# Kernel optimization log

Measured on AMD Instinct MI355X. Metric: run time of the kernel, lower is better.

Reference implementation:

```python
import jax, jax.numpy as jnp
import numpy as np

STATIC_SEQ_DIM = 48  # STAT_DIM(27) + X_TIME_DIM(13) + 8
HIDDEN = 128


def setup_inputs() -> dict:
    key = jax.random.key(0)
    ks = jax.random.split(key, 8)
    B, T = 4096, 512

    def n(k, shape, scale):
        return jax.random.normal(k, shape, dtype=jnp.float32) * scale

    return {
        "y_flow": jax.random.normal(ks[0], (B, T, 1), dtype=jnp.float32),
        "x_statics": jax.random.normal(ks[1], (B, T, STATIC_SEQ_DIM), dtype=jnp.float32),
        "twin_idx": 256,
        "enc_w1": n(ks[2], (STATIC_SEQ_DIM, STATIC_SEQ_DIM), 0.1),
        "enc_b1": jnp.zeros((STATIC_SEQ_DIM,), jnp.float32),
        "enc_w2": n(ks[3], (STATIC_SEQ_DIM, STATIC_SEQ_DIM), 0.1),
        "enc_b2": jnp.zeros((STATIC_SEQ_DIM,), jnp.float32),
        "w_ih": n(ks[4], (4 * HIDDEN, 1 + STATIC_SEQ_DIM), 0.05),
        "w_hh": n(ks[5], (4 * HIDDEN, HIDDEN), 0.05),
        "b_ih": jnp.zeros((4 * HIDDEN,), jnp.float32),
        "b_hh": jnp.zeros((4 * HIDDEN,), jnp.float32),
        "out_w": n(ks[6], (1, HIDDEN), 0.05),
        "out_b": jnp.zeros((1,), jnp.float32),
    }


def reference(y_flow, x_statics, enc_w1, enc_b1, enc_w2, enc_b2,
              w_ih, w_hh, b_ih, b_hh, out_w, out_b, twin_idx):
    B, T, _ = y_flow.shape
    H = w_hh.shape[1]
    # Static encoder MLP has no cross-time dependency -> vectorize over (B, T-1)
    xs = x_statics[:, : T - 1]                                        # (B,T-1,S)
    enc = jax.nn.relu(xs @ enc_w1.T + enc_b1) @ enc_w2.T + enc_b2     # (B,T-1,S)
    enc_t = jnp.swapaxes(enc, 0, 1)                                   # (T-1,B,S)
    flow_t = jnp.swapaxes(y_flow[:, : T - 1], 0, 1)                   # (T-1,B,1)
    ts = jnp.arange(T - 1)

    def step(carry, x):
        h, c, last_pred = carry
        flow_teacher, e_t, t = x
        flow = jnp.where(t < twin_idx - 1, flow_teacher, last_pred)   # (B,1)
        x_in = jnp.concatenate([flow, e_t], axis=-1)                  # (B,1+S)
        gates = x_in @ w_ih.T + b_ih + h @ w_hh.T + b_hh              # (B,4H)
        i, f, g, o = jnp.split(gates, 4, axis=-1)                     # torch gate order
        c_new = jax.nn.sigmoid(f) * c + jax.nn.sigmoid(i) * jnp.tanh(g)
        h_new = jax.nn.sigmoid(o) * jnp.tanh(c_new)
        pred = h_new @ out_w.T + out_b                                # (B,1)
        return (h_new, c_new, pred), pred

    h0 = jnp.zeros((B, H), jnp.float32)
    c0 = jnp.zeros((B, H), jnp.float32)
    p0 = jnp.zeros((B, 1), jnp.float32)
    _, preds = jax.lax.scan(step, (h0, c0, p0), (flow_t, enc_t, ts))  # (T-1,B,1)
    return jnp.swapaxes(preds, 0, 1)                                  # (B,T-1,1)
```

## Files before the change

kernel.cpp:

```cpp
#include <hip/hip_runtime.h>
#include <hip/hip_bf16.h>

#define HID 128
#define SDIM 48
#define NSTEP 511
#define TFULL 512
#define ROWS 16
#define XHS 200
#define O1S 88
#define WENC_OFF 98304
#define BIAS_BYTE_OFF 208896

typedef unsigned short u16;
typedef unsigned int   u32;
typedef __attribute__((ext_vector_type(8))) short short8;
typedef __attribute__((ext_vector_type(4))) float f32x4;

__device__ __forceinline__ float frcp(float x)  { return __builtin_amdgcn_rcpf(x); }
__device__ __forceinline__ float sigm(float x)  { return frcp(1.0f + __expf(-x)); }
__device__ __forceinline__ float tanh_f(float x){ return 1.0f - 2.0f*frcp(1.0f + __expf(2.0f*x)); }
__device__ __forceinline__ u16 f2bf(float f) {
  __hip_bfloat16 h = __float2bfloat16(f);
  return *reinterpret_cast<u16*>(&h);
}
__device__ __forceinline__ u32 pk2(float a, float b) {
  return (u32)f2bf(a) | ((u32)f2bf(b) << 16);
}
__device__ __forceinline__ short8 pack8(float4 a, float4 b) {
  short8 r;
  r[0]=(short)f2bf(a.x); r[1]=(short)f2bf(a.y); r[2]=(short)f2bf(a.z); r[3]=(short)f2bf(a.w);
  r[4]=(short)f2bf(b.x); r[5]=(short)f2bf(b.y); r[6]=(short)f2bf(b.z); r[7]=(short)f2bf(b.w);
  return r;
}

__global__ void setup_weights(const float* __restrict__ w_ih, const float* __restrict__ w_hh,
                              const float* __restrict__ b_ih, const float* __restrict__ b_hh,
                              const float* __restrict__ enc_w1, const float* __restrict__ enc_w2,
                              u16* __restrict__ frags, float* __restrict__ bias) {
  int stride = gridDim.x * blockDim.x;
  int i0 = blockIdx.x * blockDim.x + threadIdx.x;
  for (int idx = i0; idx < 32*6*64*8; idx += stride) {
    int j  = idx & 7;
    int l  = (idx >> 3) & 63;
    int kt = (idx >> 9) % 6;
    int mt = (idx >> 9) / 6;
    int gr = mt*16 + (l & 15);
    int k  = kt*32 + (l >> 4)*8 + j;
    float v = 0.f;
    if (k < 48)       v = w_ih[gr*49 + 1 + k];
    else if (k < 176) v = w_hh[gr*HID + (k - 48)];
    frags[idx] = f2bf(v);
  }
  for (int idx = i0; idx < 2*3*2*64*8; idx += stride) {
    int j   = idx & 7;
    int l   = (idx >> 3) & 63;
    int kt  = (idx >> 9) & 1;
    int mt  = (idx >> 10) % 3;
    int lyr = (idx >> 10) / 3;
    int row = mt*16 + (l & 15);
    int k   = kt*32 + (l >> 4)*8 + j;
    float v = 0.f;
    if (k < SDIM) v = (lyr ? enc_w2 : enc_w1)[row*SDIM + k];
    frags[WENC_OFF + idx] = f2bf(v);
  }
  for (int idx = i0; idx < 512; idx += stride)
    bias[idx] = b_ih[idx] + b_hh[idx];
}

__global__ __launch_bounds__(512, 2)
void lstm_mfma(const float* __restrict__ y_flow,
               const float* __restrict__ x_statics,
               const int* __restrict__ twin_p,
               const float* __restrict__ enc_b1, const float* __restrict__ enc_b2,
               const float* __restrict__ out_w, const float* __restrict__ out_b,
               const float* __restrict__ w_ih,
               const u16* __restrict__ frags, const float* __restrict__ bias,
               float* __restrict__ out) {
  __shared__ __attribute__((aligned(16))) u16   s_xh[2][ROWS][XHS];
  __shared__ __attribute__((aligned(16))) u16   s_o1[ROWS][O1S];
  __shared__ __attribute__((aligned(16))) float s_pp[2][ROWS][8];
  __shared__ __attribute__((aligned(16))) float s_bias[512];
  __shared__ __attribute__((aligned(16))) float s_eb1[SDIM];
  __shared__ __attribute__((aligned(16))) float s_eb2[SDIM];

  const int tid = threadIdx.x;
  const int blk = blockIdx.x;
  const int w  = tid >> 6;
  const int l  = tid & 63;
  const int lr = l & 15;
  const int lg = l >> 4;
  const size_t b0 = (size_t)blk * ROWS;

  short8 wf[4][6];
  #pragma unroll
  for (int q = 0; q < 4; ++q)
    #pragma unroll
    for (int kt = 0; kt < 6; ++kt)
      wf[q][kt] = *(const short8*)(frags + (((w + 8*q)*6 + kt)*64 + l)*8);

  float wfl[4][4];
  #pragma unroll
  for (int q = 0; q < 4; ++q)
    #pragma unroll
    for (int r = 0; r < 4; ++r)
      wfl[q][r] = w_ih[((w + 8*q)*16 + lg*4 + r)*49];

  short8 we1[3][2], we2[3][2];
  if (w == 7) {
    #pragma unroll
    for (int mt = 0; mt < 3; ++mt)
      #pragma unroll
      for (int kt = 0; kt < 2; ++kt) {
        we1[mt][kt] = *(const short8*)(frags + WENC_OFF + (((0*3 + mt)*2 + kt)*64 + l)*8);
        we2[mt][kt] = *(const short8*)(frags + WENC_OFF + (((1*3 + mt)*2 + kt)*64 + l)*8);
      }
  }

  float owv[4];
  #pragma unroll
  for (int r = 0; r < 4; ++r) owv[r] = out_w[w*16 + lg*4 + r];
  const float ob  = out_b[0];
  const int   twc = twin_p[0] - 1;

  for (int i = tid; i < 2*ROWS*XHS; i += 512) ((u16*)s_xh)[i] = 0;
  for (int i = tid; i < ROWS*O1S;  i += 512) ((u16*)s_o1)[i] = 0;
  for (int i = tid; i < 2*ROWS*8;  i += 512) ((float*)s_pp)[i] = 0.f;
  s_bias[tid] = bias[tid];
  if (tid < SDIM) { s_eb1[tid] = enc_b1[tid]; s_eb2[tid] = enc_b2[tid]; }
  __syncthreads();

  const float* xrow = x_statics + (size_t)(b0 + lr)*TFULL*SDIM;
  const float* yrow = y_flow    + (size_t)(b0 + lr)*TFULL;

  auto enc_step = [&](short8 bx0, short8 bx1, int pp) {
    f32x4 a[3];
    #pragma unroll
    for (int mt = 0; mt < 3; ++mt) a[mt] = *(const f32x4*)&s_eb1[mt*16 + lg*4];
    #pragma unroll
    for (int mt = 0; mt < 3; ++mt) {
      a[mt] = __builtin_amdgcn_mfma_f32_16x16x32_bf16(we1[mt][0], bx0, a[mt], 0, 0, 0);
      a[mt] = __builtin_amdgcn_mfma_f32_16x16x32_bf16(we1[mt][1], bx1, a[mt], 0, 0, 0);
    }
    #pragma unroll
    for (int mt = 0; mt < 3; ++mt) {
      *(u32*)&s_o1[lr][mt*16 + lg*4]     = pk2(fmaxf(a[mt][0],0.f), fmaxf(a[mt][1],0.f));
      *(u32*)&s_o1[lr][mt*16 + lg*4 + 2] = pk2(fmaxf(a[mt][2],0.f), fmaxf(a[mt][3],0.f));
    }
    asm volatile("s_waitcnt lgkmcnt(0)" ::: "memory");
    __builtin_amdgcn_sched_barrier(0);
    short8 bo0 = *(const short8*)&s_o1[lr][lg*8];
    short8 bo1 = *(const short8*)&s_o1[lr][32 + lg*8];
    f32x4 e[3];
    #pragma unroll
    for (int mt = 0; mt < 3; ++mt) e[mt] = *(const f32x4*)&s_eb2[mt*16 + lg*4];
    #pragma unroll
    for (int mt = 0; mt < 3; ++mt) {
      e[mt] = __builtin_amdgcn_mfma_f32_16x16x32_bf16(we2[mt][0], bo0, e[mt], 0, 0, 0);
      e[mt] = __builtin_amdgcn_mfma_f32_16x16x32_bf16(we2[mt][1], bo1, e[mt], 0, 0, 0);
    }
    #pragma unroll
    for (int mt = 0; mt < 3; ++mt) {
      *(u32*)&s_xh[pp][lr][mt*16 + lg*4]     = pk2(e[mt][0], e[mt][1]);
      *(u32*)&s_xh[pp][lr][mt*16 + lg*4 + 2] = pk2(e[mt][2], e[mt][3]);
    }
  };

  float4 zf4 = make_float4(0.f, 0.f, 0.f, 0.f);
  float4 xn0a = zf4, xn0b = zf4, xn1a = zf4, xn1b = zf4;
  if (w == 7) {
    float4 c0a = *(const float4*)(xrow + lg*8);
    float4 c0b = *(const float4*)(xrow + lg*8 + 4);
    float4 c1a = zf4, c1b = zf4;
    if (lg < 2) {
      c1a = *(const float4*)(xrow + 32 + lg*8);
      c1b = *(const float4*)(xrow + 32 + lg*8 + 4);
    }
    enc_step(pack8(c0a, c0b), pack8(c1a, c1b), 0);
    xn0a = *(const float4*)(xrow + SDIM + lg*8);
    xn0b = *(const float4*)(xrow + SDIM + lg*8 + 4);
    if (lg < 2) {
      xn1a = *(const float4*)(xrow + SDIM + 32 + lg*8);
      xn1b = *(const float4*)(xrow + SDIM + 32 + lg*8 + 4);
    }
  }
  float c_reg[4] = {0.f, 0.f, 0.f, 0.f};
  __syncthreads();

  for (int st = 0; st < NSTEP; ++st) {
    const int p  = st & 1;
    const int p2 = p ^ 1;

    short8 bh[6];
    #pragma unroll
    for (int kt = 0; kt < 6; ++kt)
      bh[kt] = *(const short8*)&s_xh[p][lr][kt*32 + lg*8];

    f32x4 acc[4];
    #pragma unroll
    for (int q = 0; q < 4; ++q) acc[q] = *(const f32x4*)&s_bias[(w + 8*q)*16 + lg*4];
    #pragma unroll
    for (int kt = 0; kt < 6; ++kt)
      #pragma unroll
      for (int q = 0; q < 4; ++q)
        acc[q] = __builtin_amdgcn_mfma_f32_16x16x32_bf16(wf[q][kt], bh[kt], acc[q], 0, 0, 0);

    f32x4 pa = *(const f32x4*)&s_pp[p][lr][0];
    f32x4 pb = *(const f32x4*)&s_pp[p][lr][4];
    float pp_s = ((pa[0]+pa[1]) + (pa[2]+pa[3])) + ((pb[0]+pb[1]) + (pb[2]+pb[3]));
    float pred_prev = pp_s + ob;
    if (st == 0) pred_prev = 0.f;
    if (st > 0 && l < 16 && (l >> 1) == w)
      out[(b0 + l)*NSTEP + (st - 1)] = pred_prev;

    float tf = 0.f;
    if (st < twc) tf = yrow[st];
    const float flow = (st < twc) ? tf : pred_prev;

    if (w == 7) {
      short8 bx0 = pack8(xn0a, xn0b);
      short8 bx1 = pack8(xn1a, xn1b);
      const int tt = (st + 2 < TFULL) ? (st + 2) : (TFULL - 1);
      xn0a = *(const float4*)(xrow + (size_t)tt*SDIM + lg*8);
      xn0b = *(const float4*)(xrow + (size_t)tt*SDIM + lg*8 + 4);
      if (lg < 2) {
        xn1a = *(const float4*)(xrow + (size_t)tt*SDIM + 32 + lg*8);
        xn1b = *(const float4*)(xrow + (size_t)tt*SDIM + 32 + lg*8 + 4);
      }
      __builtin_amdgcn_s_setprio(1);
      enc_step(bx0, bx1, p2);
      __builtin_amdgcn_s_setprio(0);
    }

    float hv[4];
    float hsum = 0.f;
    #pragma unroll
    for (int r = 0; r < 4; ++r) {
      float g_i = acc[0][r] + wfl[0][r]*flow;
      float g_f = acc[1][r] + wfl[1][r]*flow;
      float g_g = acc[2][r] + wfl[2][r]*flow;
      float g_o = acc[3][r] + wfl[3][r]*flow;
      float iv = sigm(g_i);
      float fv = sigm(g_f);
      float gv = tanh_f(g_g);
      float ov = sigm(g_o);
      float c  = fv*c_reg[r] + iv*gv;
      c_reg[r] = c;
      hv[r] = ov*tanh_f(c);
      hsum += hv[r]*owv[r];
    }
    *(u32*)&s_xh[p2][lr][48 + w*16 + lg*4]     = pk2(hv[0], hv[1]);
    *(u32*)&s_xh[p2][lr][48 + w*16 + lg*4 + 2] = pk2(hv[2], hv[3]);
    hsum += __shfl_xor(hsum, 16);
    hsum += __shfl_xor(hsum, 32);
    if (l < 16) s_pp[p2][l][w] = hsum;
    __syncthreads();
  }

  f32x4 pa = *(const f32x4*)&s_pp[NSTEP & 1][lr][0];
  f32x4 pb = *(const f32x4*)&s_pp[NSTEP & 1][lr][4];
  float pp_s = ((pa[0]+pa[1]) + (pa[2]+pa[3])) + ((pb[0]+pb[1]) + (pb[2]+pb[3]));
  if (l < 16 && (l >> 1) == w)
    out[(b0 + l)*NSTEP + (NSTEP - 1)] = pp_s + ob;
}

extern "C" void kernel_launch(void* const* d_in, const int* in_sizes, int n_in,
                              void* d_out, int out_size, void* d_ws, size_t ws_size,
                              hipStream_t stream) {
  const float* y_flow    = (const float*)d_in[0];
  const float* x_statics = (const float*)d_in[1];
  const int*   twin      = (const int*)  d_in[2];
  const float* enc_w1    = (const float*)d_in[3];
  const float* enc_b1    = (const float*)d_in[4];
  const float* enc_w2    = (const float*)d_in[5];
  const float* enc_b2    = (const float*)d_in[6];
  const float* w_ih      = (const float*)d_in[7];
  const float* w_hh      = (const float*)d_in[8];
  const float* b_ih      = (const float*)d_in[9];
  const float* b_hh      = (const float*)d_in[10];
  const float* out_w     = (const float*)d_in[11];
  const float* out_b     = (const float*)d_in[12];
  float* out = (float*)d_out;

  char* ws = (char*)d_ws;
  u16*   frags = (u16*)ws;
  float* bias  = (float*)(ws + BIAS_BYTE_OFF);

  setup_weights<<<128, 256, 0, stream>>>(w_ih, w_hh, b_ih, b_hh, enc_w1, enc_w2, frags, bias);
  lstm_mfma<<<256, 512, 0, stream>>>(y_flow, x_statics, twin,
                                     enc_b1, enc_b2, out_w, out_b, w_ih,
                                     frags, bias, out);
}
```

Baseline: 802.4 us.

## Split static encoder across two waves and break MFMA accumulator chains

Encoder layer 1 moves to wave 6 and layer 2 to wave 7, with a double-buffered intermediate between them, so the encoder runs as a two-stage pipeline. This takes the serialized two-layer MLP off a single wave's critical path in each recurrent step. The gate GEMM now splits the K loop into two independent accumulator sets, which shortens the dependent MFMA chain at the cost of extra adds and registers. The prediction partial sums are also transposed to a [wave][row] layout, and the enc_L1 parameter named `ob` shadows the outer out_b variable of the same name.

```diff
diff --git a/kernel.cpp b/kernel.cpp
--- a/kernel.cpp
+++ b/kernel.cpp
@@ -77,8 +77,8 @@
                const u16* __restrict__ frags, const float* __restrict__ bias,
                float* __restrict__ out) {
   __shared__ __attribute__((aligned(16))) u16   s_xh[2][ROWS][XHS];
-  __shared__ __attribute__((aligned(16))) u16   s_o1[ROWS][O1S];
-  __shared__ __attribute__((aligned(16))) float s_pp[2][ROWS][8];
+  __shared__ __attribute__((aligned(16))) u16   s_o1[2][ROWS][O1S];
+  __shared__ __attribute__((aligned(16))) float s_pp[2][8][ROWS];
   __shared__ __attribute__((aligned(16))) float s_bias[512];
   __shared__ __attribute__((aligned(16))) float s_eb1[SDIM];
   __shared__ __attribute__((aligned(16))) float s_eb2[SDIM];
@@ -106,7 +106,7 @@
       wfl[q][r] = w_ih[((w + 8*q)*16 + lg*4 + r)*49];
 
   short8 we1[3][2], we2[3][2];
-  if (w == 7) {
+  if (w >= 6) {
     #pragma unroll
     for (int mt = 0; mt < 3; ++mt)
       #pragma unroll
@@ -123,8 +123,8 @@
   const int   twc = twin_p[0] - 1;
 
   for (int i = tid; i < 2*ROWS*XHS; i += 512) ((u16*)s_xh)[i] = 0;
-  for (int i = tid; i < ROWS*O1S;  i += 512) ((u16*)s_o1)[i] = 0;
-  for (int i = tid; i < 2*ROWS*8;  i += 512) ((float*)s_pp)[i] = 0.f;
+  for (int i = tid; i < 2*ROWS*O1S; i += 512) ((u16*)s_o1)[i] = 0;
+  for (int i = tid; i < 2*8*ROWS;  i += 512) ((float*)s_pp)[i] = 0.f;
   s_bias[tid] = bias[tid];
   if (tid < SDIM) { s_eb1[tid] = enc_b1[tid]; s_eb2[tid] = enc_b2[tid]; }
   __syncthreads();
@@ -132,7 +132,7 @@
   const float* xrow = x_statics + (size_t)(b0 + lr)*TFULL*SDIM;
   const float* yrow = y_flow    + (size_t)(b0 + lr)*TFULL;
 
-  auto enc_step = [&](short8 bx0, short8 bx1, int pp) {
+  auto enc_L1 = [&](short8 bx0, short8 bx1, int ob) {
     f32x4 a[3];
     #pragma unroll
     for (int mt = 0; mt < 3; ++mt) a[mt] = *(const f32x4*)&s_eb1[mt*16 + lg*4];
@@ -143,13 +143,13 @@
     }
     #pragma unroll
     for (int mt = 0; mt < 3; ++mt) {
-      *(u32*)&s_o1[lr][mt*16 + lg*4]     = pk2(fmaxf(a[mt][0],0.f), fmaxf(a[mt][1],0.f));
-      *(u32*)&s_o1[lr][mt*16 + lg*4 + 2] = pk2(fmaxf(a[mt][2],0.f), fmaxf(a[mt][3],0.f));
-    }
-    asm volatile("s_waitcnt lgkmcnt(0)" ::: "memory");
-    __builtin_amdgcn_sched_barrier(0);
-    short8 bo0 = *(const short8*)&s_o1[lr][lg*8];
-    short8 bo1 = *(const short8*)&s_o1[lr][32 + lg*8];
+      *(u32*)&s_o1[ob][lr][mt*16 + lg*4]     = pk2(fmaxf(a[mt][0],0.f), fmaxf(a[mt][1],0.f));
+      *(u32*)&s_o1[ob][lr][mt*16 + lg*4 + 2] = pk2(fmaxf(a[mt][2],0.f), fmaxf(a[mt][3],0.f));
+    }
+  };
+  auto enc_L2 = [&](int ib, int pp) {
+    short8 bo0 = *(const short8*)&s_o1[ib][lr][lg*8];
+    short8 bo1 = *(const short8*)&s_o1[ib][lr][32 + lg*8];
     f32x4 e[3];
     #pragma unroll
     for (int mt = 0; mt < 3; ++mt) e[mt] = *(const f32x4*)&s_eb2[mt*16 + lg*4];
@@ -164,24 +164,30 @@
       *(u32*)&s_xh[pp][lr][mt*16 + lg*4 + 2] = pk2(e[mt][2], e[mt][3]);
     }
   };
+  auto load_xs = [&](int t, float4& a0, float4& b0_, float4& a1, float4& b1_) {
+    a0 = *(const float4*)(xrow + (size_t)t*SDIM + lg*8);
+    b0_= *(const float4*)(xrow + (size_t)t*SDIM + lg*8 + 4);
+    if (lg < 2) {
+      a1 = *(const float4*)(xrow + (size_t)t*SDIM + 32 + lg*8);
+      b1_= *(const float4*)(xrow + (size_t)t*SDIM + 32 + lg*8 + 4);
+    }
+  };
 
   float4 zf4 = make_float4(0.f, 0.f, 0.f, 0.f);
   float4 xn0a = zf4, xn0b = zf4, xn1a = zf4, xn1b = zf4;
   if (w == 7) {
-    float4 c0a = *(const float4*)(xrow + lg*8);
-    float4 c0b = *(const float4*)(xrow + lg*8 + 4);
-    float4 c1a = zf4, c1b = zf4;
-    if (lg < 2) {
-      c1a = *(const float4*)(xrow + 32 + lg*8);
-      c1b = *(const float4*)(xrow + 32 + lg*8 + 4);
-    }
-    enc_step(pack8(c0a, c0b), pack8(c1a, c1b), 0);
-    xn0a = *(const float4*)(xrow + SDIM + lg*8);
-    xn0b = *(const float4*)(xrow + SDIM + lg*8 + 4);
-    if (lg < 2) {
-      xn1a = *(const float4*)(xrow + SDIM + 32 + lg*8);
-      xn1b = *(const float4*)(xrow + SDIM + 32 + lg*8 + 4);
-    }
+    float4 c0a = zf4, c0b = zf4, c1a = zf4, c1b = zf4;
+    load_xs(0, c0a, c0b, c1a, c1b);
+    enc_L1(pack8(c0a, c0b), pack8(c1a, c1b), 0);
+    asm volatile("s_waitcnt lgkmcnt(0)" ::: "memory");
+    __builtin_amdgcn_sched_barrier(0);
+    enc_L2(0, 0);
+  }
+  if (w == 6) {
+    float4 c0a = zf4, c0b = zf4, c1a = zf4, c1b = zf4;
+    load_xs(1, c0a, c0b, c1a, c1b);
+    enc_L1(pack8(c0a, c0b), pack8(c1a, c1b), 1);
+    load_xs(2, xn0a, xn0b, xn1a, xn1b);
   }
   float c_reg[4] = {0.f, 0.f, 0.f, 0.f};
   __syncthreads();
@@ -195,19 +201,40 @@
     for (int kt = 0; kt < 6; ++kt)
       bh[kt] = *(const short8*)&s_xh[p][lr][kt*32 + lg*8];
 
-    f32x4 acc[4];
-    #pragma unroll
-    for (int q = 0; q < 4; ++q) acc[q] = *(const f32x4*)&s_bias[(w + 8*q)*16 + lg*4];
-    #pragma unroll
-    for (int kt = 0; kt < 6; ++kt)
+    f32x4 accA[4], accB[4];
+    #pragma unroll
+    for (int q = 0; q < 4; ++q) {
+      accA[q] = *(const f32x4*)&s_bias[(w + 8*q)*16 + lg*4];
+      accB[q] = (f32x4){0.f, 0.f, 0.f, 0.f};
+    }
+    #pragma unroll
+    for (int kt = 0; kt < 3; ++kt)
       #pragma unroll
-      for (int q = 0; q < 4; ++q)
-        acc[q] = __builtin_amdgcn_mfma_f32_16x16x32_bf16(wf[q][kt], bh[kt], acc[q], 0, 0, 0);
-
-    f32x4 pa = *(const f32x4*)&s_pp[p][lr][0];
-    f32x4 pb = *(const f32x4*)&s_pp[p][lr][4];
-    float pp_s = ((pa[0]+pa[1]) + (pa[2]+pa[3])) + ((pb[0]+pb[1]) + (pb[2]+pb[3]));
-    float pred_prev = pp_s + ob;
+      for (int q = 0; q < 4; ++q) {
+        accA[q] = __builtin_amdgcn_mfma_f32_16x16x32_bf16(wf[q][kt],   bh[kt],   accA[q], 0, 0, 0);
+        accB[q] = __builtin_amdgcn_mfma_f32_16x16x32_bf16(wf[q][kt+3], bh[kt+3], accB[q], 0, 0, 0);
+      }
+
+    if (w == 6) {
+      short8 bx0 = pack8(xn0a, xn0b);
+      short8 bx1 = pack8(xn1a, xn1b);
+      const int tt = (st + 3 < TFULL) ? (st + 3) : (TFULL - 1);
+      load_xs(tt, xn0a, xn0b, xn1a, xn1b);
+      __builtin_amdgcn_s_setprio(1);
+      enc_L1(bx0, bx1, st & 1);
+      __builtin_amdgcn_s_setprio(0);
+    }
+    if (w == 7) {
+      __builtin_amdgcn_s_setprio(1);
+      enc_L2((st + 1) & 1, p2);
+      __builtin_amdgcn_s_setprio(0);
+    }
+
+    float pp01 = s_pp[p][0][lr] + s_pp[p][1][lr];
+    float pp23 = s_pp[p][2][lr] + s_pp[p][3][lr];
+    float pp45 = s_pp[p][4][lr] + s_pp[p][5][lr];
+    float pp67 = s_pp[p][6][lr] + s_pp[p][7][lr];
+    float pred_prev = ((pp01 + pp23) + (pp45 + pp67)) + ob;
     if (st == 0) pred_prev = 0.f;
     if (st > 0 && l < 16 && (l >> 1) == w)
       out[(b0 + l)*NSTEP + (st - 1)] = pred_prev;
@@ -216,29 +243,14 @@
     if (st < twc) tf = yrow[st];
     const float flow = (st < twc) ? tf : pred_prev;
 
-    if (w == 7) {
-      short8 bx0 = pack8(xn0a, xn0b);
-      short8 bx1 = pack8(xn1a, xn1b);
-      const int tt = (st + 2 < TFULL) ? (st + 2) : (TFULL - 1);
-      xn0a = *(const float4*)(xrow + (size_t)tt*SDIM + lg*8);
-      xn0b = *(const float4*)(xrow + (size_t)tt*SDIM + lg*8 + 4);
-      if (lg < 2) {
-        xn1a = *(const float4*)(xrow + (size_t)tt*SDIM + 32 + lg*8);
-        xn1b = *(const float4*)(xrow + (size_t)tt*SDIM + 32 + lg*8 + 4);
-      }
-      __builtin_amdgcn_s_setprio(1);
-      enc_step(bx0, bx1, p2);
-      __builtin_amdgcn_s_setprio(0);
-    }
-
     float hv[4];
     float hsum = 0.f;
     #pragma unroll
     for (int r = 0; r < 4; ++r) {
-      float g_i = acc[0][r] + wfl[0][r]*flow;
-      float g_f = acc[1][r] + wfl[1][r]*flow;
-      float g_g = acc[2][r] + wfl[2][r]*flow;
-      float g_o = acc[3][r] + wfl[3][r]*flow;
+      float g_i = (accA[0][r] + accB[0][r]) + wfl[0][r]*flow;
+      float g_f = (accA[1][r] + accB[1][r]) + wfl[1][r]*flow;
+      float g_g = (accA[2][r] + accB[2][r]) + wfl[2][r]*flow;
+      float g_o = (accA[3][r] + accB[3][r]) + wfl[3][r]*flow;
       float iv = sigm(g_i);
       float fv = sigm(g_f);
       float gv = tanh_f(g_g);
@@ -252,15 +264,17 @@
     *(u32*)&s_xh[p2][lr][48 + w*16 + lg*4 + 2] = pk2(hv[2], hv[3]);
     hsum += __shfl_xor(hsum, 16);
     hsum += __shfl_xor(hsum, 32);
-    if (l < 16) s_pp[p2][l][w] = hsum;
+    if (l < 16) s_pp[p2][w][l] = hsum;
     __syncthreads();
   }
 
-  f32x4 pa = *(const f32x4*)&s_pp[NSTEP & 1][lr][0];
-  f32x4 pb = *(const f32x4*)&s_pp[NSTEP & 1][lr][4];
-  float pp_s = ((pa[0]+pa[1]) + (pa[2]+pa[3])) + ((pb[0]+pb[1]) + (pb[2]+pb[3]));
+  const int pe = NSTEP & 1;
+  float pp01 = s_pp[pe][0][lr] + s_pp[pe][1][lr];
+  float pp23 = s_pp[pe][2][lr] + s_pp[pe][3][lr];
+  float pp45 = s_pp[pe][4][lr] + s_pp[pe][5][lr];
+  float pp67 = s_pp[pe][6][lr] + s_pp[pe][7][lr];
   if (l < 16 && (l >> 1) == w)
-    out[(b0 + l)*NSTEP + (NSTEP - 1)] = pp_s + ob;
+    out[(b0 + l)*NSTEP + (NSTEP - 1)] = ((pp01 + pp23) + (pp45 + pp67)) + ob;
 }
 
 extern "C" void kernel_launch(void* const* d_in, const int* in_sizes, int n_in,
```

After: 903.2 us. +12.6%, slower.

## Precompute static encoder in separate parallel kernel, stream bf16 encodings into LSTM

Applied to the files above, without the earlier changes.

Adds an enc_pre kernel that runs the two-layer static encoder MLP for all (batch, time) positions in parallel and writes bf16 results to a workspace buffer. The recurrent kernel then loads each step's encoding straight into MFMA B-fragments from global memory, instead of having one wave compute the encoder inside the serial loop. Weight fragments are reordered so the hidden state comes first, and the shared buffers shrink. This takes encoder work off the critical serial path. The cost is an extra kernel and a large bf16 workspace round-trip, with a fallback path kept for when the workspace is too small.

```diff
diff --git a/kernel.cpp b/kernel.cpp
--- a/kernel.cpp
+++ b/kernel.cpp
@@ -7,9 +7,12 @@
 #define TFULL 512
 #define ROWS 16
 #define XHS 200
+#define HSTR 136
 #define O1S 88
 #define WENC_OFF 98304
 #define BIAS_BYTE_OFF 208896
+#define ENC_BYTE_OFF 211200
+#define ENC_BYTES (4096ULL*TFULL*SDIM*2ULL)
 
 typedef unsigned short u16;
 typedef unsigned int   u32;
@@ -36,7 +39,7 @@
 __global__ void setup_weights(const float* __restrict__ w_ih, const float* __restrict__ w_hh,
                               const float* __restrict__ b_ih, const float* __restrict__ b_hh,
                               const float* __restrict__ enc_w1, const float* __restrict__ enc_w2,
-                              u16* __restrict__ frags, float* __restrict__ bias) {
+                              u16* __restrict__ frags, float* __restrict__ bias, int hfirst) {
   int stride = gridDim.x * blockDim.x;
   int i0 = blockIdx.x * blockDim.x + threadIdx.x;
   for (int idx = i0; idx < 32*6*64*8; idx += stride) {
@@ -47,8 +50,13 @@
     int gr = mt*16 + (l & 15);
     int k  = kt*32 + (l >> 4)*8 + j;
     float v = 0.f;
-    if (k < 48)       v = w_ih[gr*49 + 1 + k];
-    else if (k < 176) v = w_hh[gr*HID + (k - 48)];
+    if (hfirst) {
+      if (k < HID)       v = w_hh[gr*HID + k];
+      else if (k < 176)  v = w_ih[gr*49 + 1 + (k - HID)];
+    } else {
+      if (k < 48)        v = w_ih[gr*49 + 1 + k];
+      else if (k < 176)  v = w_hh[gr*HID + (k - 48)];
+    }
     frags[idx] = f2bf(v);
   }
   for (int idx = i0; idx < 2*3*2*64*8; idx += stride) {
@@ -67,21 +75,85 @@
     bias[idx] = b_ih[idx] + b_hh[idx];
 }
 
+__global__ __launch_bounds__(256)
+void enc_pre(const float* __restrict__ x_statics,
+             const float* __restrict__ enc_b1, const float* __restrict__ enc_b2,
+             const u16* __restrict__ frags, u16* __restrict__ enc_buf) {
+  __shared__ __attribute__((aligned(16))) u16 s_o1[4][ROWS][O1S];
+  const int tid = threadIdx.x;
+  const int w  = tid >> 6;
+  const int l  = tid & 63;
+  const int lr = l & 15;
+  const int lg = l >> 4;
+  const int b     = blockIdx.x >> 3;
+  const int chunk = blockIdx.x & 7;
+  const int t = chunk*64 + w*16 + lr;
+
+  short8 we1[3][2], we2[3][2];
+  f32x4 a[3], e[3];
+  #pragma unroll
+  for (int mt = 0; mt < 3; ++mt) {
+    #pragma unroll
+    for (int kt = 0; kt < 2; ++kt) {
+      we1[mt][kt] = *(const short8*)(frags + WENC_OFF + (((0*3 + mt)*2 + kt)*64 + l)*8);
+      we2[mt][kt] = *(const short8*)(frags + WENC_OFF + (((1*3 + mt)*2 + kt)*64 + l)*8);
+    }
+    a[mt] = *(const f32x4*)&enc_b1[mt*16 + lg*4];
+    e[mt] = *(const f32x4*)&enc_b2[mt*16 + lg*4];
+  }
+
+  *(unsigned long long*)&s_o1[w][l & 15][48 + (l >> 4)*4] = 0ULL;
+
+  const float* xbase = x_statics + ((size_t)b*TFULL + t)*SDIM;
+  float4 zf4 = make_float4(0.f,0.f,0.f,0.f);
+  float4 c0a = *(const float4*)(xbase + lg*8);
+  float4 c0b = *(const float4*)(xbase + lg*8 + 4);
+  float4 c1a = zf4, c1b = zf4;
+  if (lg < 2) {
+    c1a = *(const float4*)(xbase + 32 + lg*8);
+    c1b = *(const float4*)(xbase + 32 + lg*8 + 4);
+  }
+  short8 bx0 = pack8(c0a, c0b);
+  short8 bx1 = pack8(c1a, c1b);
+
+  #pragma unroll
+  for (int mt = 0; mt < 3; ++mt) {
+    a[mt] = __builtin_amdgcn_mfma_f32_16x16x32_bf16(we1[mt][0], bx0, a[mt], 0, 0, 0);
+    a[mt] = __builtin_amdgcn_mfma_f32_16x16x32_bf16(we1[mt][1], bx1, a[mt], 0, 0, 0);
+  }
+  #pragma unroll
+  for (int mt = 0; mt < 3; ++mt) {
+    u32 lo = pk2(fmaxf(a[mt][0],0.f), fmaxf(a[mt][1],0.f));
+    u32 hi = pk2(fmaxf(a[mt][2],0.f), fmaxf(a[mt][3],0.f));
+    *(uint2*)&s_o1[w][lr][mt*16 + lg*4] = make_uint2(lo, hi);
+  }
+  asm volatile("s_waitcnt lgkmcnt(0)" ::: "memory");
+  __builtin_amdgcn_sched_barrier(0);
+  short8 bo0 = *(const short8*)&s_o1[w][lr][lg*8];
+  short8 bo1 = *(const short8*)&s_o1[w][lr][32 + lg*8];
+  #pragma unroll
+  for (int mt = 0; mt < 3; ++mt) {
+    e[mt] = __builtin_amdgcn_mfma_f32_16x16x32_bf16(we2[mt][0], bo0, e[mt], 0, 0, 0);
+    e[mt] = __builtin_amdgcn_mfma_f32_16x16x32_bf16(we2[mt][1], bo1, e[mt], 0, 0, 0);
+  }
+  if (t < NSTEP) {
+    u16* dst = enc_buf + ((size_t)b*TFULL + t)*SDIM;
+    #pragma unroll
+    for (int mt = 0; mt < 3; ++mt)
+      *(uint2*)(dst + mt*16 + lg*4) = make_uint2(pk2(e[mt][0], e[mt][1]), pk2(e[mt][2], e[mt][3]));
+  }
+}
+
 __global__ __launch_bounds__(512, 2)
-void lstm_mfma(const float* __restrict__ y_flow,
-               const float* __restrict__ x_statics,
-               const int* __restrict__ twin_p,
-               const float* __restrict__ enc_b1, const float* __restrict__ enc_b2,
-               const float* __restrict__ out_w, const float* __restrict__ out_b,
-               const float* __restrict__ w_ih,
-               const u16* __restrict__ frags, const float* __restrict__ bias,
-               float* __restrict__ out) {
-  __shared__ __attribute__((aligned(16))) u16   s_xh[2][ROWS][XHS];
-  __shared__ __attribute__((aligned(16))) u16   s_o1[ROWS][O1S];
-  __shared__ __attribute__((aligned(16))) float s_pp[2][ROWS][8];
-  __shared__ __attribute__((aligned(16))) float s_bias[512];
-  __shared__ __attribute__((aligned(16))) float s_eb1[SDIM];
-  __shared__ __attribute__((aligned(16))) float s_eb2[SDIM];
+void lstm_pre(const float* __restrict__ y_flow,
+              const int* __restrict__ twin_p,
+              const float* __restrict__ out_w, const float* __restrict__ out_b,
+              const float* __restrict__ w_ih,
+              const u16* __restrict__ frags, const float* __restrict__ bias,
+              const u16* __restrict__ enc_buf,
+              float* __restrict__ out) {
+  __shared__ __attribute__((aligned(16))) u16   s_h[2][ROWS][HSTR];
+  __shared__ __attribute__((aligned(16))) float s_pp[2][8][ROWS];
 
   const int tid = threadIdx.x;
   const int blk = blockIdx.x;
@@ -105,6 +177,139 @@
     for (int r = 0; r < 4; ++r)
       wfl[q][r] = w_ih[((w + 8*q)*16 + lg*4 + r)*49];
 
+  f32x4 bgv[4];
+  #pragma unroll
+  for (int q = 0; q < 4; ++q)
+    bgv[q] = *(const f32x4*)&bias[(w + 8*q)*16 + lg*4];
+
+  float owv[4];
+  #pragma unroll
+  for (int r = 0; r < 4; ++r) owv[r] = out_w[w*16 + lg*4 + r];
+  const float ob  = out_b[0];
+  const int   twc = twin_p[0] - 1;
+
+  const u16*   erow = enc_buf + (size_t)(b0 + lr)*TFULL*SDIM;
+  const float* yrow = y_flow  + (size_t)(b0 + lr)*TFULL;
+
+  short8 encA = *(const short8*)(erow + lg*8);
+  short8 encB = {};
+  if (lg < 2) encB = *(const short8*)(erow + 32 + lg*8);
+
+  for (int i = tid; i < 2*ROWS*HSTR; i += 512) ((u16*)s_h)[i] = 0;
+  for (int i = tid; i < 2*8*ROWS;   i += 512) ((float*)s_pp)[i] = 0.f;
+  float c_reg[4] = {0.f, 0.f, 0.f, 0.f};
+  __syncthreads();
+
+  for (int st = 0; st < NSTEP; ++st) {
+    const int p  = st & 1;
+    const int p2 = p ^ 1;
+
+    short8 bh[6];
+    #pragma unroll
+    for (int kt = 0; kt < 4; ++kt)
+      bh[kt] = *(const short8*)&s_h[p][lr][kt*32 + lg*8];
+    bh[4] = encA;
+    bh[5] = encB;
+
+    float tf = 0.f;
+    if (st < twc) tf = yrow[st];
+
+    const int tt = (st + 1 < NSTEP) ? (st + 1) : (NSTEP - 1);
+    encA = *(const short8*)(erow + (size_t)tt*SDIM + lg*8);
+    encB = (short8){};
+    if (lg < 2) encB = *(const short8*)(erow + (size_t)tt*SDIM + 32 + lg*8);
+
+    f32x4 acc[4];
+    #pragma unroll
+    for (int q = 0; q < 4; ++q) acc[q] = bgv[q];
+    #pragma unroll
+    for (int kt = 0; kt < 6; ++kt)
+      #pragma unroll
+      for (int q = 0; q < 4; ++q)
+        acc[q] = __builtin_amdgcn_mfma_f32_16x16x32_bf16(wf[q][kt], bh[kt], acc[q], 0, 0, 0);
+
+    float pp01 = s_pp[p][0][lr] + s_pp[p][1][lr];
+    float pp23 = s_pp[p][2][lr] + s_pp[p][3][lr];
+    float pp45 = s_pp[p][4][lr] + s_pp[p][5][lr];
+    float pp67 = s_pp[p][6][lr] + s_pp[p][7][lr];
+    float pred_prev = ((pp01 + pp23) + (pp45 + pp67)) + ob;
+    if (st == 0) pred_prev = 0.f;
+    if (st > 0 && l < 16 && (l >> 1) == w)
+      out[(b0 + l)*NSTEP + (st - 1)] = pred_prev;
+
+    const float flow = (st < twc) ? tf : pred_prev;
+
+    float hv[4];
+    float hsum = 0.f;
+    #pragma unroll
+    for (int r = 0; r < 4; ++r) {
+      float g_i = acc[0][r] + wfl[0][r]*flow;
+      float g_f = acc[1][r] + wfl[1][r]*flow;
+      float g_g = acc[2][r] + wfl[2][r]*flow;
+      float g_o = acc[3][r] + wfl[3][r]*flow;
+      float iv = sigm(g_i);
+      float fv = sigm(g_f);
+      float gv = tanh_f(g_g);
+      float ov = sigm(g_o);
+      float c  = fv*c_reg[r] + iv*gv;
+      c_reg[r] = c;
+      hv[r] = ov*tanh_f(c);
+      hsum += hv[r]*owv[r];
+    }
+    *(uint2*)&s_h[p2][lr][w*16 + lg*4] = make_uint2(pk2(hv[0], hv[1]), pk2(hv[2], hv[3]));
+    hsum += __shfl_xor(hsum, 16);
+    hsum += __shfl_xor(hsum, 32);
+    if (l < 16) s_pp[p2][w][l] = hsum;
+    __syncthreads();
+  }
+
+  const int pe = NSTEP & 1;
+  float pp01 = s_pp[pe][0][lr] + s_pp[pe][1][lr];
+  float pp23 = s_pp[pe][2][lr] + s_pp[pe][3][lr];
+  float pp45 = s_pp[pe][4][lr] + s_pp[pe][5][lr];
+  float pp67 = s_pp[pe][6][lr] + s_pp[pe][7][lr];
+  if (l < 16 && (l >> 1) == w)
+    out[(b0 + l)*NSTEP + (NSTEP - 1)] = ((pp01 + pp23) + (pp45 + pp67)) + ob;
+}
+
+__global__ __launch_bounds__(512, 2)
+void lstm_fb(const float* __restrict__ y_flow,
+             const float* __restrict__ x_statics,
+             const int* __restrict__ twin_p,
+             const float* __restrict__ enc_b1, const float* __restrict__ enc_b2,
+             const float* __restrict__ out_w, const float* __restrict__ out_b,
+             const float* __restrict__ w_ih,
+             const u16* __restrict__ frags, const float* __restrict__ bias,
+             float* __restrict__ out) {
+  __shared__ __attribute__((aligned(16))) u16   s_xh[2][ROWS][XHS];
+  __shared__ __attribute__((aligned(16))) u16   s_o1[ROWS][O1S];
+  __shared__ __attribute__((aligned(16))) float s_pp[2][ROWS][8];
+  __shared__ __attribute__((aligned(16))) float s_bias[512];
+  __shared__ __attribute__((aligned(16))) float s_eb1[SDIM];
+  __shared__ __attribute__((aligned(16))) float s_eb2[SDIM];
+
+  const int tid = threadIdx.x;
+  const int blk = blockIdx.x;
+  const int w  = tid >> 6;
+  const int l  = tid & 63;
+  const int lr = l & 15;
+  const int lg = l >> 4;
+  const size_t b0 = (size_t)blk * ROWS;
+
+  short8 wf[4][6];
+  #pragma unroll
+  for (int q = 0; q < 4; ++q)
+    #pragma unroll
+    for (int kt = 0; kt < 6; ++kt)
+      wf[q][kt] = *(const short8*)(frags + (((w + 8*q)*6 + kt)*64 + l)*8);
+
+  float wfl[4][4];
+  #pragma unroll
+  for (int q = 0; q < 4; ++q)
+    #pragma unroll
+    for (int r = 0; r < 4; ++r)
+      wfl[q][r] = w_ih[((w + 8*q)*16 + lg*4 + r)*49];
+
   short8 we1[3][2], we2[3][2];
   if (w == 7) {
     #pragma unroll
@@ -164,24 +369,22 @@
       *(u32*)&s_xh[pp][lr][mt*16 + lg*4 + 2] = pk2(e[mt][2], e[mt][3]);
     }
   };
+  auto load_xs = [&](int t, float4& a0, float4& b0_, float4& a1, float4& b1_) {
+    a0 = *(const float4*)(xrow + (size_t)t*SDIM + lg*8);
+    b0_= *(const float4*)(xrow + (size_t)t*SDIM + lg*8 + 4);
+    if (lg < 2) {
+      a1 = *(const float4*)(xrow + (size_t)t*SDIM + 32 + lg*8);
+      b1_= *(const float4*)(xrow + (size_t)t*SDIM + 32 + lg*8 + 4);
+    }
+  };
 
   float4 zf4 = make_float4(0.f, 0.f, 0.f, 0.f);
   float4 xn0a = zf4, xn0b = zf4, xn1a = zf4, xn1b = zf4;
   if (w == 7) {
-    float4 c0a = *(const float4*)(xrow + lg*8);
-    float4 c0b = *(const float4*)(xrow + lg*8 + 4);
-    float4 c1a = zf4, c1b = zf4;
-    if (lg < 2) {
-      c1a = *(const float4*)(xrow + 32 + lg*8);
-      c1b = *(const float4*)(xrow + 32 + lg*8 + 4);
-    }
+    float4 c0a = zf4, c0b = zf4, c1a = zf4, c1b = zf4;
+    load_xs(0, c0a, c0b, c1a, c1b);
     enc_step(pack8(c0a, c0b), pack8(c1a, c1b), 0);
-    xn0a = *(const float4*)(xrow + SDIM + lg*8);
-    xn0b = *(const float4*)(xrow + SDIM + lg*8 + 4);
-    if (lg < 2) {
-      xn1a = *(const float4*)(xrow + SDIM + 32 + lg*8);
-      xn1b = *(const float4*)(xrow + SDIM + 32 + lg*8 + 4);
-    }
+    load_xs(1, xn0a, xn0b, xn1a, xn1b);
   }
   float c_reg[4] = {0.f, 0.f, 0.f, 0.f};
   __syncthreads();
@@ -220,12 +423,7 @@
       short8 bx0 = pack8(xn0a, xn0b);
       short8 bx1 = pack8(xn1a, xn1b);
       const int tt = (st + 2 < TFULL) ? (st + 2) : (TFULL - 1);
-      xn0a = *(const float4*)(xrow + (size_t)tt*SDIM + lg*8);
-      xn0b = *(const float4*)(xrow + (size_t)tt*SDIM + lg*8 + 4);
-      if (lg < 2) {
-        xn1a = *(const float4*)(xrow + (size_t)tt*SDIM + 32 + lg*8);
-        xn1b = *(const float4*)(xrow + (size_t)tt*SDIM + 32 + lg*8 + 4);
-      }
+      load_xs(tt, xn0a, xn0b, xn1a, xn1b);
       __builtin_amdgcn_s_setprio(1);
       enc_step(bx0, bx1, p2);
       __builtin_amdgcn_s_setprio(0);
@@ -282,11 +480,21 @@
   float* out = (float*)d_out;
 
   char* ws = (char*)d_ws;
-  u16*   frags = (u16*)ws;
-  float* bias  = (float*)(ws + BIAS_BYTE_OFF);
-
-  setup_weights<<<128, 256, 0, stream>>>(w_ih, w_hh, b_ih, b_hh, enc_w1, enc_w2, frags, bias);
-  lstm_mfma<<<256, 512, 0, stream>>>(y_flow, x_statics, twin,
+  u16*   frags   = (u16*)ws;
+  float* bias    = (float*)(ws + BIAS_BYTE_OFF);
+  u16*   enc_buf = (u16*)(ws + ENC_BYTE_OFF);
+
+  const int pre = (ws_size >= (size_t)ENC_BYTE_OFF + ENC_BYTES) ? 1 : 0;
+
+  setup_weights<<<128, 256, 0, stream>>>(w_ih, w_hh, b_ih, b_hh, enc_w1, enc_w2,
+                                         frags, bias, pre);
+  if (pre) {
+    enc_pre<<<4096*8, 256, 0, stream>>>(x_statics, enc_b1, enc_b2, frags, enc_buf);
+    lstm_pre<<<256, 512, 0, stream>>>(y_flow, twin, out_w, out_b, w_ih,
+                                      frags, bias, enc_buf, out);
+  } else {
+    lstm_fb<<<256, 512, 0, stream>>>(y_flow, x_statics, twin,
                                      enc_b1, enc_b2, out_w, out_b, w_ih,
                                      frags, bias, out);
-}
+  }
+}
```

After: 901.3 us. 12.3% more time.
